# Optimization experiments

Measured on AMD Instinct MI355X. Metric: run time of the kernel, lower is better.

Reference implementation:

```python
import jax, jax.numpy as jnp
import numpy as np

GRAPH_NUM = 2
HOP_K = 2
NODE_EMB_DIM = 16
INPUT_DIM = 2
HIDDEN = 64
B, N = 8, 400
IN_FEAT = INPUT_DIM + HIDDEN                      # 66, input to each MetaDGCN
I_DIM = (GRAPH_NUM * HOP_K + 1) * IN_FEAT         # 330


def setup_inputs() -> dict:
    key = jax.random.key(0)
    ks = jax.random.split(key, 8)
    x = jax.random.normal(ks[0], (B, N, INPUT_DIM), dtype=jnp.float32)
    state = jax.random.normal(ks[1], (B, N, HIDDEN), dtype=jnp.float32)
    graphs = jax.random.uniform(ks[2], (GRAPH_NUM, B, N, N), dtype=jnp.float32)
    # row-normalize like asym_adj so message passing is stable
    graphs = graphs / graphs.sum(-1, keepdims=True)
    node_emb = jax.random.normal(ks[3], (B, N, NODE_EMB_DIM), dtype=jnp.float32)
    s = 1.0 / np.sqrt(I_DIM)
    Wg = jax.random.normal(ks[4], (NODE_EMB_DIM, I_DIM, 2 * HIDDEN), dtype=jnp.float32) * s
    bg = jax.random.normal(ks[5], (NODE_EMB_DIM, 2 * HIDDEN), dtype=jnp.float32) * 0.1
    Wc = jax.random.normal(ks[6], (NODE_EMB_DIM, I_DIM, HIDDEN), dtype=jnp.float32) * s
    bc = jax.random.normal(ks[7], (NODE_EMB_DIM, HIDDEN), dtype=jnp.float32) * 0.1
    return {"x": x, "state": state, "graphs": graphs, "node_emb": node_emb,
            "Wg": Wg, "bg": bg, "Wc": Wc, "bc": bc}


def meta_dgcn(x, graphs, node_emb, weights_pool, bias_pool):
    # multi-hop propagation over each dynamic graph (GCN: 'bnm,bmd->bnd')
    out = [x]
    for i in range(GRAPH_NUM):
        x1 = x
        for _ in range(HOP_K):
            x1 = jnp.einsum('bnm,bmd->bnd', graphs[i], x1)
            out.append(x1)
    h = jnp.concatenate(out, axis=-1)                          # [B,N,I_DIM]
    # meta-generated per-node weights and bias
    weights = jnp.einsum('bnd,dio->bnio', node_emb, weights_pool)  # [B,N,I,O]
    bias = jnp.einsum('bnd,do->bno', node_emb, bias_pool)
    return jnp.einsum('bni,bnio->bno', h, weights) + bias


def reference(x, state, graphs, node_emb, Wg, bg, Wc, bc):
    # GRU-style meta-graph recurrent cell (MetaDGCRU)
    xs = jnp.concatenate([x, state], axis=-1)                  # [B,N,IN_FEAT]
    zr = jax.nn.sigmoid(meta_dgcn(xs, graphs, node_emb, Wg, bg))
    z, r = jnp.split(zr, 2, axis=-1)
    xrs = jnp.concatenate([x, r * state], axis=-1)
    hc = jnp.tanh(meta_dgcn(xrs, graphs, node_emb, Wc, bc))
    h = z * state + (1.0 - z) * hc                             # [B,N,HIDDEN]
    return h
```

## Files before the change

kernel.cpp:

```cpp
#include <hip/hip_runtime.h>
#include <hip/hip_bf16.h>
#include <math.h>

#define Bb 8
#define Nn 400
#define GN 2
#define INF 66
#define IDIM 330
#define KP 352
#define HID 64
#define EMB 16
#define NKP 416
#define XTR 80
constexpr int M = Bb * Nn;

typedef __attribute__((ext_vector_type(8))) short short8;
typedef __attribute__((ext_vector_type(4))) float f32x4;

__device__ __forceinline__ ushort f2bf(float f) {
    union { float f; unsigned u; } v; v.f = f;
    unsigned u = v.u;
    unsigned r = (u + 0x7FFFu + ((u >> 16) & 1u)) >> 16;
    return (ushort)r;
}

#define GBLKS4 2600
__global__ void k_prep(const float* __restrict__ G, const float* __restrict__ Wg,
                       const float* __restrict__ Wc, const float* __restrict__ x,
                       const float* __restrict__ state,
                       ushort* __restrict__ Gbf, ushort* __restrict__ WgT,
                       ushort* __restrict__ WcT, ushort* __restrict__ Hbf,
                       ushort* __restrict__ XTin) {
    __shared__ float Tw[32][65];
    __shared__ ushort Tc[64][XTR + 1];
    int bid = blockIdx.x;
    if (bid < GBLKS4) {
        size_t tid4 = ((size_t)bid * 256 + threadIdx.x) * 4;
        int k = (int)(tid4 % NKP);
        size_t row = tid4 / NKP;
        ushort4 o;
        if (k < Nn) {
            float4 gv = *(const float4*)(G + row * Nn + k);
            o.x = f2bf(gv.x); o.y = f2bf(gv.y); o.z = f2bf(gv.z); o.w = f2bf(gv.w);
        } else {
            o.x = o.y = o.z = o.w = 0;
        }
        *(ushort4*)(Gbf + tid4) = o;
        return;
    }
    bid -= GBLKS4;
    if (bid < 352 + 176) {
        const float* W; ushort* WT; int O;
        if (bid < 352) { W = Wg; WT = WgT; O = 128; }
        else           { bid -= 352; W = Wc; WT = WcT; O = 64; }
        const int k0 = (bid % 11) * 32;
        const int c0 = (bid / 11) * 64;
        const int d = c0 / O, o0 = c0 % O;
        for (int e = threadIdx.x; e < 2048; e += 256) {
            int kk = e >> 6, oo = e & 63;
            int k = k0 + kk;
            Tw[kk][oo] = (k < IDIM) ? W[((size_t)d * IDIM + k) * O + o0 + oo] : 0.f;
        }
        __syncthreads();
        for (int e = threadIdx.x; e < 2048; e += 256) {
            int cc = e >> 5, kk = e & 31;
            WT[(size_t)(c0 + cc) * KP + k0 + kk] = f2bf(Tw[kk][cc]);
        }
        return;
    }
    bid -= 528;
    const int b = bid / 7;
    const int k0 = (bid % 7) * 64;
    for (int e = threadIdx.x; e < 64 * XTR; e += 256) {
        int kk = e / XTR, c = e % XTR;
        int k = k0 + kk;
        ushort bf = 0;
        if (k < Nn && c < INF) {
            float v = (c < 2) ? x[((size_t)b * Nn + k) * 2 + c]
                              : state[((size_t)b * Nn + k) * HID + c - 2];
            bf = f2bf(v);
            Hbf[((size_t)b * Nn + k) * KP + c] = bf;
        }
        Tc[kk][c] = bf;
    }
    for (int e = threadIdx.x; e < 64 * 22; e += 256) {
        int kk = e / 22, c = 330 + e % 22;
        int k = k0 + kk;
        if (k < Nn) Hbf[((size_t)b * Nn + k) * KP + c] = 0;
    }
    __syncthreads();
    for (int e = threadIdx.x; e < XTR * 64; e += 256) {
        int c = e / 64, kk = e % 64;
        int k = k0 + kk;
        if (k < NKP) XTin[((size_t)b * XTR + c) * NKP + k] = Tc[kk][c];
    }
}

__global__ __launch_bounds__(256) void k_hop(const ushort* __restrict__ Gbf,
                      const ushort* __restrict__ XT,
                      ushort* __restrict__ Hb, ushort* __restrict__ XTnext,
                      int out_base, int xt_per_g) {
    const int b = blockIdx.y, g = blockIdx.z;
    const int row0 = blockIdx.x * 16;
    const int wid = threadIdx.x >> 6, lane = threadIdx.x & 63;
    const int lr = lane & 15, kq = lane >> 4;
    __shared__ float Red[3][5][256];

    const ushort* Gb = Gbf + (size_t)(g * Bb + b) * Nn * NKP;
    const ushort* Xb = XT + (size_t)((xt_per_g ? g * Bb : 0) + b) * XTR * NKP;
    const ushort* Grow = Gb + (size_t)(row0 + lr) * NKP;

    f32x4 acc[5] = {};
#pragma unroll
    for (int i = 0; i < 4; ++i) {
        const int ks = i * 4 + wid;
        if (ks < 13) {
            short8 af = *(const short8*)(Grow + ks * 32 + kq * 8);
#pragma unroll
            for (int n = 0; n < 5; ++n) {
                short8 bv = *(const short8*)(Xb + (size_t)(n * 16 + lr) * NKP + ks * 32 + kq * 8);
                acc[n] = __builtin_amdgcn_mfma_f32_16x16x32_bf16(af, bv, acc[n], 0, 0, 0);
            }
        }
    }

    if (wid) {
#pragma unroll
        for (int n = 0; n < 5; ++n)
#pragma unroll
            for (int r = 0; r < 4; ++r)
                Red[wid - 1][n][(kq * 4 + r) * 16 + lr] = acc[n][r];
    }
    __syncthreads();
    if (wid == 0) {
#pragma unroll
        for (int n = 0; n < 5; ++n)
#pragma unroll
            for (int r = 0; r < 4; ++r) {
                const int idx = (kq * 4 + r) * 16 + lr;
                acc[n][r] += Red[0][n][idx] + Red[1][n][idx] + Red[2][n][idx];
            }
        const int rbase = row0 + kq * 4;
        ushort* Hout = Hb + (size_t)b * Nn * KP + out_base + g * 132;
#pragma unroll
        for (int n = 0; n < 5; ++n) {
            int col = n * 16 + lr;
            if (col < INF) {
#pragma unroll
                for (int r = 0; r < 4; ++r)
                    Hout[(size_t)(rbase + r) * KP + col] = f2bf(acc[n][r]);
            }
        }
        if (XTnext) {
            ushort* Xn = XTnext + (size_t)(g * Bb + b) * XTR * NKP;
#pragma unroll
            for (int n = 0; n < 5; ++n) {
                int col = n * 16 + lr;
                ushort4 w;
#pragma unroll
                for (int r = 0; r < 4; ++r)
                    w[r] = (col < INF) ? f2bf(acc[n][r]) : (ushort)0;
                *(ushort4*)(Xn + (size_t)col * NKP + rbase) = w;
            }
        }
    }
}

template <int O>
__global__ __launch_bounds__(256, 3) void k_meta_fused(const ushort* __restrict__ Hbf,
        const ushort* __restrict__ WT, const float* __restrict__ emb,
        float* __restrict__ P) {
    constexpr int NB = O / 32;
    constexpr int PB = O / 64;
    __shared__ ushort As[2][64][40];
    __shared__ ushort Bs[2][2][O][40];
    const int ds = blockIdx.x;
    const int bm = blockIdx.y * 64;
    const int t = threadIdx.x;
    const int wid = t >> 6, lane = t & 63;
    const int wm = wid >> 1, wn = wid & 1;
    const int lr = lane & 15, kq = lane >> 4;

    const int ar = t >> 2, akc = (t & 3) * 8;
    const ushort* srcA = Hbf + (size_t)(bm + ar) * KP + akc;
    const ushort* srcB[2][PB];
    int brow[PB], bkc[PB];
#pragma unroll
    for (int p = 0; p < PB; ++p) {
        int chunk = t + p * 256;
        brow[p] = chunk >> 2; bkc[p] = (chunk & 3) * 8;
#pragma unroll
        for (int j = 0; j < 2; ++j)
            srcB[j][p] = WT + ((size_t)(ds * 2 + j) * O + brow[p]) * KP + bkc[p];
    }

    short8 ra, rb[2][PB];
    ra = *(const short8*)srcA;
#pragma unroll
    for (int j = 0; j < 2; ++j)
#pragma unroll
        for (int p = 0; p < PB; ++p) rb[j][p] = *(const short8*)srcB[j][p];

    f32x4 seg[2][2][NB] = {};

    for (int ks = 0; ks < 11; ++ks) {
        const int buf = ks & 1;
        *(short8*)&As[buf][ar][akc] = ra;
#pragma unroll
        for (int j = 0; j < 2; ++j)
#pragma unroll
            for (int p = 0; p < PB; ++p) *(short8*)&Bs[buf][j][brow[p]][bkc[p]] = rb[j][p];
        if (ks < 10) {
            const int k0 = (ks + 1) * 32;
            ra = *(const short8*)(srcA + k0);
#pragma unroll
            for (int j = 0; j < 2; ++j)
#pragma unroll
                for (int p = 0; p < PB; ++p) rb[j][p] = *(const short8*)(srcB[j][p] + k0);
        }
        __syncthreads();
        short8 a[2], bf[2][NB];
#pragma unroll
        for (int m = 0; m < 2; ++m)
            a[m] = *(const short8*)&As[buf][wm * 32 + m * 16 + lr][kq * 8];
#pragma unroll
        for (int j = 0; j < 2; ++j)
#pragma unroll
            for (int n = 0; n < NB; ++n)
                bf[j][n] = *(const short8*)&Bs[buf][j][wn * (O / 2) + n * 16 + lr][kq * 8];
#pragma unroll
        for (int j = 0; j < 2; ++j)
#pragma unroll
            for (int m = 0; m < 2; ++m)
#pragma unroll
                for (int n = 0; n < NB; ++n)
                    seg[j][m][n] = __builtin_amdgcn_mfma_f32_16x16x32_bf16(a[m], bf[j][n], seg[j][m][n], 0, 0, 0);
    }

    float* Pd = P + (size_t)ds * M * O;
#pragma unroll
    for (int m = 0; m < 2; ++m) {
        const int rbase = bm + wm * 32 + m * 16 + kq * 4;
#pragma unroll
        for (int r = 0; r < 4; ++r) {
            const int row = rbase + r;
            float e0 = emb[(size_t)row * EMB + ds * 2];
            float e1 = emb[(size_t)row * EMB + ds * 2 + 1];
#pragma unroll
            for (int n = 0; n < NB; ++n) {
                const int col = wn * (O / 2) + n * 16 + lr;
                Pd[(size_t)row * O + col] = e0 * seg[0][m][n][r] + e1 * seg[1][m][n][r];
            }
        }
    }
}

__global__ void k_zr(const float* __restrict__ P, const float* __restrict__ emb,
                     const float* __restrict__ bg, const float* __restrict__ state,
                     float* __restrict__ zbuf, ushort* __restrict__ Hbf,
                     ushort* __restrict__ XTin) {
    __shared__ float es[2][EMB];
    const int t = threadIdx.x;
    if (t < 2 * EMB) es[t >> 4][t & 15] = emb[((size_t)blockIdx.x * 2 + (t >> 4)) * EMB + (t & 15)];
    __syncthreads();
    const int node = blockIdx.x * 2 + (t >> 7);
    const int o = t & 127;
    float v = 0.f;
#pragma unroll
    for (int s = 0; s < 8; ++s) v += P[((size_t)s * M + node) * 128 + o];
    const float* e_ = es[t >> 7];
#pragma unroll
    for (int d = 0; d < EMB; ++d) v += e_[d] * bg[d * 128 + o];
    float sg = 1.f / (1.f + expf(-v));
    if (o < 64) {
        zbuf[node * 64 + o] = sg;
    } else {
        int oo = o - 64;
        ushort bf = f2bf(sg * state[node * 64 + oo]);
        Hbf[(size_t)node * KP + 2 + oo] = bf;
        int b = node / Nn, kn = node % Nn;
        XTin[((size_t)b * XTR + 2 + oo) * NKP + kn] = bf;
    }
}

__global__ void k_final(const float* __restrict__ P, const float* __restrict__ emb,
                        const float* __restrict__ bc, const float* __restrict__ zbuf,
                        const float* __restrict__ state, float* __restrict__ out) {
    __shared__ float es[4][EMB];
    const int t = threadIdx.x;
    if (t < 4 * EMB) es[t >> 4][t & 15] = emb[((size_t)blockIdx.x * 4 + (t >> 4)) * EMB + (t & 15)];
    __syncthreads();
    const int node = blockIdx.x * 4 + (t >> 6);
    const int o = t & 63;
    float v = 0.f;
#pragma unroll
    for (int s = 0; s < 8; ++s) v += P[((size_t)s * M + node) * 64 + o];
    const float* e_ = es[t >> 6];
#pragma unroll
    for (int d = 0; d < EMB; ++d) v += e_[d] * bc[d * 64 + o];
    float hc = tanhf(v);
    float z = zbuf[node * 64 + o];
    out[node * 64 + o] = z * state[node * 64 + o] + (1.f - z) * hc;
}

extern "C" void kernel_launch(void* const* d_in, const int* in_sizes, int n_in,
                              void* d_out, int out_size, void* d_ws, size_t ws_size,
                              hipStream_t stream) {
    const float* x      = (const float*)d_in[0];
    const float* state  = (const float*)d_in[1];
    const float* graphs = (const float*)d_in[2];
    const float* emb    = (const float*)d_in[3];
    const float* Wg     = (const float*)d_in[4];
    const float* bg     = (const float*)d_in[5];
    const float* Wc     = (const float*)d_in[6];
    const float* bc     = (const float*)d_in[7];
    float* out = (float*)d_out;

    char* ws = (char*)d_ws;
    ushort* Hbf  = (ushort*)ws;  ws += (size_t)M * KP * 2;
    ushort* Gbf  = (ushort*)ws;  ws += (size_t)GN * Bb * Nn * NKP * 2;
    ushort* WgT  = (ushort*)ws;  ws += (size_t)2048 * KP * 2;
    ushort* WcT  = (ushort*)ws;  ws += (size_t)1024 * KP * 2;
    ushort* XTin = (ushort*)ws;  ws += (size_t)Bb * XTR * NKP * 2;
    ushort* XTmid= (ushort*)ws;  ws += (size_t)GN * Bb * XTR * NKP * 2;
    float*  PG   = (float*)ws;   ws += (size_t)8 * M * 128 * 4;
    float*  PC   = (float*)ws;   ws += (size_t)8 * M * 64 * 4;
    float*  zb   = (float*)ws;

    dim3 hopgrid(25, Bb, GN);

    k_prep<<<3184, 256, 0, stream>>>(graphs, Wg, Wc, x, state, Gbf, WgT, WcT, Hbf, XTin);

    k_hop<<<hopgrid, 256, 0, stream>>>(Gbf, XTin, Hbf, XTmid, 66, 0);
    k_hop<<<hopgrid, 256, 0, stream>>>(Gbf, XTmid, Hbf, nullptr, 132, 1);
    k_meta_fused<128><<<dim3(8, 50), 256, 0, stream>>>(Hbf, WgT, emb, PG);
    k_zr<<<1600, 256, 0, stream>>>(PG, emb, bg, state, zb, Hbf, XTin);

    k_hop<<<hopgrid, 256, 0, stream>>>(Gbf, XTin, Hbf, XTmid, 66, 0);
    k_hop<<<hopgrid, 256, 0, stream>>>(Gbf, XTmid, Hbf, nullptr, 132, 1);
    k_meta_fused<64><<<dim3(8, 50), 256, 0, stream>>>(Hbf, WcT, emb, PC);
    k_final<<<800, 256, 0, stream>>>(PC, emb, bc, zb, state, out);
}
```

Baseline: 77.16 us.

## Use single-wave hop blocks and split gate meta-GEMM per embedding dim

```diff
diff --git a/kernel.cpp b/kernel.cpp
--- a/kernel.cpp
+++ b/kernel.cpp
@@ -96,15 +96,14 @@
     }
 }
 
-__global__ __launch_bounds__(256) void k_hop(const ushort* __restrict__ Gbf,
+__global__ __launch_bounds__(64) void k_hop(const ushort* __restrict__ Gbf,
                       const ushort* __restrict__ XT,
                       ushort* __restrict__ Hb, ushort* __restrict__ XTnext,
                       int out_base, int xt_per_g) {
     const int b = blockIdx.y, g = blockIdx.z;
     const int row0 = blockIdx.x * 16;
-    const int wid = threadIdx.x >> 6, lane = threadIdx.x & 63;
+    const int lane = threadIdx.x;
     const int lr = lane & 15, kq = lane >> 4;
-    __shared__ float Red[3][5][256];
 
     const ushort* Gb = Gbf + (size_t)(g * Bb + b) * Nn * NKP;
     const ushort* Xb = XT + (size_t)((xt_per_g ? g * Bb : 0) + b) * XTR * NKP;
@@ -112,55 +111,109 @@
 
     f32x4 acc[5] = {};
 #pragma unroll
-    for (int i = 0; i < 4; ++i) {
-        const int ks = i * 4 + wid;
-        if (ks < 13) {
-            short8 af = *(const short8*)(Grow + ks * 32 + kq * 8);
-#pragma unroll
-            for (int n = 0; n < 5; ++n) {
-                short8 bv = *(const short8*)(Xb + (size_t)(n * 16 + lr) * NKP + ks * 32 + kq * 8);
-                acc[n] = __builtin_amdgcn_mfma_f32_16x16x32_bf16(af, bv, acc[n], 0, 0, 0);
-            }
-        }
-    }
-
-    if (wid) {
-#pragma unroll
-        for (int n = 0; n < 5; ++n)
+    for (int ks = 0; ks < 13; ++ks) {
+        short8 af = *(const short8*)(Grow + ks * 32 + kq * 8);
+#pragma unroll
+        for (int n = 0; n < 5; ++n) {
+            short8 bv = *(const short8*)(Xb + (size_t)(n * 16 + lr) * NKP + ks * 32 + kq * 8);
+            acc[n] = __builtin_amdgcn_mfma_f32_16x16x32_bf16(af, bv, acc[n], 0, 0, 0);
+        }
+    }
+
+    const int rbase = row0 + kq * 4;
+    ushort* Hout = Hb + (size_t)b * Nn * KP + out_base + g * 132;
+#pragma unroll
+    for (int n = 0; n < 5; ++n) {
+        int col = n * 16 + lr;
+        if (col < INF) {
 #pragma unroll
             for (int r = 0; r < 4; ++r)
-                Red[wid - 1][n][(kq * 4 + r) * 16 + lr] = acc[n][r];
-    }
-    __syncthreads();
-    if (wid == 0) {
-#pragma unroll
-        for (int n = 0; n < 5; ++n)
-#pragma unroll
-            for (int r = 0; r < 4; ++r) {
-                const int idx = (kq * 4 + r) * 16 + lr;
-                acc[n][r] += Red[0][n][idx] + Red[1][n][idx] + Red[2][n][idx];
-            }
-        const int rbase = row0 + kq * 4;
-        ushort* Hout = Hb + (size_t)b * Nn * KP + out_base + g * 132;
+                Hout[(size_t)(rbase + r) * KP + col] = f2bf(acc[n][r]);
+        }
+    }
+    if (XTnext) {
+        ushort* Xn = XTnext + (size_t)(g * Bb + b) * XTR * NKP;
 #pragma unroll
         for (int n = 0; n < 5; ++n) {
             int col = n * 16 + lr;
-            if (col < INF) {
-#pragma unroll
-                for (int r = 0; r < 4; ++r)
-                    Hout[(size_t)(rbase + r) * KP + col] = f2bf(acc[n][r]);
-            }
-        }
-        if (XTnext) {
-            ushort* Xn = XTnext + (size_t)(g * Bb + b) * XTR * NKP;
-#pragma unroll
-            for (int n = 0; n < 5; ++n) {
-                int col = n * 16 + lr;
-                ushort4 w;
-#pragma unroll
-                for (int r = 0; r < 4; ++r)
-                    w[r] = (col < INF) ? f2bf(acc[n][r]) : (ushort)0;
-                *(ushort4*)(Xn + (size_t)col * NKP + rbase) = w;
+            ushort4 w;
+#pragma unroll
+            for (int r = 0; r < 4; ++r)
+                w[r] = (col < INF) ? f2bf(acc[n][r]) : (ushort)0;
+            *(ushort4*)(Xn + (size_t)col * NKP + rbase) = w;
+        }
+    }
+}
+
+__global__ __launch_bounds__(256, 4) void k_meta_d16(const ushort* __restrict__ Hbf,
+        const ushort* __restrict__ WT, const float* __restrict__ emb,
+        float* __restrict__ P) {
+    constexpr int O = 128;
+    __shared__ ushort As[2][64][40];
+    __shared__ ushort Bs[2][O][40];
+    const int d = blockIdx.x;
+    const int bm = blockIdx.y * 64;
+    const int t = threadIdx.x;
+    const int wid = t >> 6, lane = t & 63;
+    const int wm = wid >> 1, wn = wid & 1;
+    const int lr = lane & 15, kq = lane >> 4;
+
+    const int ar = t >> 2, akc = (t & 3) * 8;
+    const ushort* srcA = Hbf + (size_t)(bm + ar) * KP + akc;
+    int brow[2], bkc[2];
+    const ushort* srcB[2];
+#pragma unroll
+    for (int p = 0; p < 2; ++p) {
+        int chunk = t + p * 256;
+        brow[p] = chunk >> 2; bkc[p] = (chunk & 3) * 8;
+        srcB[p] = WT + ((size_t)d * O + brow[p]) * KP + bkc[p];
+    }
+
+    short8 ra, rb[2];
+    ra = *(const short8*)srcA;
+#pragma unroll
+    for (int p = 0; p < 2; ++p) rb[p] = *(const short8*)srcB[p];
+
+    f32x4 seg[2][4] = {};
+
+    for (int ks = 0; ks < 11; ++ks) {
+        const int buf = ks & 1;
+        *(short8*)&As[buf][ar][akc] = ra;
+#pragma unroll
+        for (int p = 0; p < 2; ++p) *(short8*)&Bs[buf][brow[p]][bkc[p]] = rb[p];
+        if (ks < 10) {
+            const int k0 = (ks + 1) * 32;
+            ra = *(const short8*)(srcA + k0);
+#pragma unroll
+            for (int p = 0; p < 2; ++p) rb[p] = *(const short8*)(srcB[p] + k0);
+        }
+        __syncthreads();
+        short8 a[2], bf[4];
+#pragma unroll
+        for (int m = 0; m < 2; ++m)
+            a[m] = *(const short8*)&As[buf][wm * 32 + m * 16 + lr][kq * 8];
+#pragma unroll
+        for (int n = 0; n < 4; ++n)
+            bf[n] = *(const short8*)&Bs[buf][wn * 64 + n * 16 + lr][kq * 8];
+#pragma unroll
+        for (int m = 0; m < 2; ++m)
+#pragma unroll
+            for (int n = 0; n < 4; ++n)
+                seg[m][n] = __builtin_amdgcn_mfma_f32_16x16x32_bf16(a[m], bf[n], seg[m][n], 0, 0, 0);
+    }
+
+    float* Pd = P + (size_t)d * M * O;
+#pragma unroll
+    for (int m = 0; m < 2; ++m) {
+        const int rbase = bm + wm * 32 + m * 16 + kq * 4;
+#pragma unroll
+        for (int r = 0; r < 4; ++r) {
+            const int row = rbase + r;
+            float e0 = emb[(size_t)row * EMB + d];
+#pragma unroll
+            for (int n = 0; n < 4; ++n) {
+                const int col = wn * 64 + n * 16 + lr;
+                Pd[(size_t)row * O + col] = e0 * seg[m][n][r];
             }
         }
     }
@@ -267,7 +320,7 @@
     const int o = t & 127;
     float v = 0.f;
 #pragma unroll
-    for (int s = 0; s < 8; ++s) v += P[((size_t)s * M + node) * 128 + o];
+    for (int s = 0; s < 16; ++s) v += P[((size_t)s * M + node) * 128 + o];
     const float* e_ = es[t >> 7];
 #pragma unroll
     for (int d = 0; d < EMB; ++d) v += e_[d] * bg[d * 128 + o];
@@ -323,7 +376,7 @@
     ushort* WcT  = (ushort*)ws;  ws += (size_t)1024 * KP * 2;
     ushort* XTin = (ushort*)ws;  ws += (size_t)Bb * XTR * NKP * 2;
     ushort* XTmid= (ushort*)ws;  ws += (size_t)GN * Bb * XTR * NKP * 2;
-    float*  PG   = (float*)ws;   ws += (size_t)8 * M * 128 * 4;
+    float*  PG   = (float*)ws;   ws += (size_t)16 * M * 128 * 4;
     float*  PC   = (float*)ws;   ws += (size_t)8 * M * 64 * 4;
     float*  zb   = (float*)ws;
 
@@ -331,13 +384,13 @@
 
     k_prep<<<3184, 256, 0, stream>>>(graphs, Wg, Wc, x, state, Gbf, WgT, WcT, Hbf, XTin);
 
-    k_hop<<<hopgrid, 256, 0, stream>>>(Gbf, XTin, Hbf, XTmid, 66, 0);
-    k_hop<<<hopgrid, 256, 0, stream>>>(Gbf, XTmid, Hbf, nullptr, 132, 1);
-    k_meta_fused<128><<<dim3(8, 50), 256, 0, stream>>>(Hbf, WgT, emb, PG);
+    k_hop<<<hopgrid, 64, 0, stream>>>(Gbf, XTin, Hbf, XTmid, 66, 0);
+    k_hop<<<hopgrid, 64, 0, stream>>>(Gbf, XTmid, Hbf, nullptr, 132, 1);
+    k_meta_d16<<<dim3(16, 50), 256, 0, stream>>>(Hbf, WgT, emb, PG);
     k_zr<<<1600, 256, 0, stream>>>(PG, emb, bg, state, zb, Hbf, XTin);
 
-    k_hop<<<hopgrid, 256, 0, stream>>>(Gbf, XTin, Hbf, XTmid, 66, 0);
-    k_hop<<<hopgrid, 256, 0, stream>>>(Gbf, XTmid, Hbf, nullptr, 132, 1);
+    k_hop<<<hopgrid, 64, 0, stream>>>(Gbf, XTin, Hbf, XTmid, 66, 0);
+    k_hop<<<hopgrid, 64, 0, stream>>>(Gbf, XTmid, Hbf, nullptr, 132, 1);
     k_meta_fused<64><<<dim3(8, 50), 256, 0, stream>>>(Hbf, WcT, emb, PC);
     k_final<<<800, 256, 0, stream>>>(PC, emb, bc, zb, state, out);
 }
```

Result: faster. 73.76 us (median of 2 runs) (-4.4%).
